# Kernel tuning notes

Measured on AMD Instinct MI355X. Metric: run time of the kernel, lower is better.

Reference implementation:

```python
import jax, jax.numpy as jnp
import numpy as np
from jax import lax

EPS = 1e-8

def int8_fq(x):
    # Int8ActPerTensorFloat: per-tensor float scale from runtime max-abs, fake-quant with STE.
    s = jnp.maximum(jnp.max(jnp.abs(x)) / 127.0, EPS)
    q = jnp.clip(jnp.round(x / s), -128.0, 127.0) * s
    return x + lax.stop_gradient(q - x)

def bin_w(w):
    # BINARY weight quant: per-tensor scale = mean(|w|), weights -> +/- scale (STE).
    s = jnp.mean(jnp.abs(w))
    wq = jnp.where(w >= 0, s, -s)
    return w + lax.stop_gradient(wq - w)

def qrelu(x):
    # QuantReLU with int8 input_quant and int8 act_quant
    return int8_fq(jax.nn.relu(int8_fq(x)))

def conv2d(x, w, b):
    y = lax.conv_general_dilated(x, w, window_strides=(1, 1), padding='VALID',
                                 dimension_numbers=('NCHW', 'OIHW', 'NCHW'))
    return y + b[None, :, None, None]

def maxpool2(x):
    return lax.reduce_window(x, -jnp.inf, lax.max, (1, 1, 2, 2), (1, 1, 2, 2), 'VALID')

def setup_inputs() -> dict:
    key = jax.random.key(0)
    ks = jax.random.split(key, 12)
    B = 16384
    inp = {
        'input_tensor': jax.random.normal(ks[0], (B, 3, 32, 32), dtype=jnp.float32),
        'w1': jax.random.normal(ks[1], (6, 3, 5, 5), dtype=jnp.float32) * 0.1,
        'b1': jax.random.normal(ks[2], (6,), dtype=jnp.float32) * 0.01,
        'w2': jax.random.normal(ks[3], (16, 6, 5, 5), dtype=jnp.float32) * 0.1,
        'b2': jax.random.normal(ks[4], (16,), dtype=jnp.float32) * 0.01,
        'fw1': jax.random.normal(ks[5], (120, 400), dtype=jnp.float32) * 0.05,
        'fb1': jax.random.normal(ks[6], (120,), dtype=jnp.float32) * 0.01,
        'fw2': jax.random.normal(ks[7], (84, 120), dtype=jnp.float32) * 0.05,
        'fb2': jax.random.normal(ks[8], (84,), dtype=jnp.float32) * 0.01,
        'fw3': jax.random.normal(ks[9], (10, 84), dtype=jnp.float32) * 0.05,
        'fb3': jax.random.normal(ks[10], (10,), dtype=jnp.float32) * 0.01,
    }
    return inp

def reference(input_tensor, w1, b1, w2, b2, fw1, fb1, fw2, fb2, fw3, fb3):
    x = int8_fq(input_tensor)                  # QuantIdentity
    x = qrelu(conv2d(x, bin_w(w1), b1))        # conv1 + relu1: [B,6,28,28]
    x = maxpool2(x)                            # [B,6,14,14]
    x = qrelu(conv2d(x, bin_w(w2), b2))        # conv2 + relu2: [B,16,10,10]
    x = maxpool2(x)                            # [B,16,5,5]
    x = x.reshape(x.shape[0], -1)              # [B,400]
    x = qrelu(x @ bin_w(fw1).T + fb1)          # fc1 + relu3: [B,120]
    x = qrelu(x @ bin_w(fw2).T + fb2)          # fc2 + relu4: [B,84]
    out = x @ bin_w(fw3).T + fb3               # fc3: [B,10]
    return out
```

## Files before the change

### kernel.cpp

```cpp
#include <hip/hip_runtime.h>
#include <math.h>

#define BATCH 16384
#define EPSQ 1e-8f

#define OFF_SCAL 0
#define OFF_WPK1 16
#define OFF_WPK2 196
#define OFF_FQ1  1156
#define OFF_FQ2  13156
#define OFF_FQ3  15844
#define OFF_A    16384
#define OFF_QIN   OFF_A
#define OFF_QC2   OFF_A
#define OFF_ISUM2 (OFF_A + 6400000)
#define OFF_QC3   (OFF_A + 10000000)
#define OFF_P3    (OFF_A + 12000000)
#define OFF_P4    (OFF_A + 14000000)
#define OFF_ISUM1 (OFF_A + 18874368)

__device__ inline int sdot4(unsigned int a, unsigned int b, int c) {
    return __builtin_amdgcn_sdot4((int)a, (int)b, c, false);
}

__device__ inline unsigned int fkey(float f) {
    unsigned int u = __float_as_uint(f);
    return (u & 0x80000000u) ? ~u : (u | 0x80000000u);
}
__device__ inline float fdec(unsigned int k) {
    unsigned int u = (k & 0x80000000u) ? (k ^ 0x80000000u) : ~k;
    return __uint_as_float(u);
}
#define KEY_ZERO   0x80000000u
#define KEY_NEGINF 0x007FFFFFu

__device__ inline float waveMax(float v) {
    #pragma unroll
    for (int off = 32; off > 0; off >>= 1)
        v = fmaxf(v, __shfl_down(v, off, 64));
    return v;
}

__device__ inline void blockAtomicMax2(float vmax, float vnmax,
                                       unsigned int* gmax, unsigned int* gnmax) {
    __shared__ float sm[4], sn[4];
    float a = waveMax(vmax), b = waveMax(vnmax);
    int tid = threadIdx.x;
    if ((tid & 63) == 0) { sm[tid >> 6] = a; sn[tid >> 6] = b; }
    __syncthreads();
    if (tid == 0) {
        atomicMax(gmax, fkey(fmaxf(fmaxf(sm[0], sm[1]), fmaxf(sm[2], sm[3]))));
        atomicMax(gnmax, fkey(fmaxf(fmaxf(sn[0], sn[1]), fmaxf(sn[2], sn[3]))));
    }
}

__device__ inline float fq_elem(float x, float s) {
    float q = fminf(fmaxf(rintf(x / s), -128.0f), 127.0f);
    return q * s;
}
__device__ inline int qrelu_code(float x, float s1, float s2) {
    float q = fq_elem(x, s1);
    q = fmaxf(q, 0.0f);
    return (int)fminf(fmaxf(rintf(q / s2), -128.0f), 127.0f);
}
__device__ inline void get_qrelu_scales(const unsigned int* scalu, int slot,
                                        float& s1, float& s2) {
    float maxa = fdec(scalu[slot]), negm = fdec(scalu[slot + 1]);
    float absm = fmaxf(maxa, negm);
    s1 = fmaxf(absm / 127.0f, EPSQ);
    float qm = fminf(fmaxf(rintf(maxa / s1), -128.0f), 127.0f) * s1;
    s2 = fmaxf(fmaxf(qm, 0.0f) / 127.0f, EPSQ);
}

__device__ inline unsigned int sgn8(float w) { return (w >= 0.0f) ? 0x01u : 0xFFu; }

__device__ inline unsigned int u32at(const unsigned int* wv, int wi, int k) {
    return (k == 0) ? wv[wi]
        : __builtin_amdgcn_perm(wv[wi + 1], wv[wi], 0x03020100u + 0x01010101u * (unsigned)k);
}

__global__ __launch_bounds__(256) void prep_kernel(const float* __restrict__ w1,
        const float* __restrict__ w2, const float* __restrict__ fw1,
        const float* __restrict__ fw2, const float* __restrict__ fw3,
        float* __restrict__ wsf) {
    int blk = blockIdx.x, tid = threadIdx.x;
    unsigned int* wsu = (unsigned int*)wsf;
    if (blk == 0) {
        if (tid == 0) wsu[0] = KEY_ZERO;
        else if (tid <= 8) wsu[tid] = KEY_NEGINF;
        return;
    }
    const float* src = nullptr; int N = 0;
    if (blk == 1)      { src = w1;  N = 450; }
    else if (blk == 2) { src = w2;  N = 2400; }
    else if (blk == 3) { src = fw1; N = 48000; }
    else if (blk == 4) { src = fw2; N = 10080; }
    else               { src = fw3; N = 840; }
    __shared__ float red[256];
    float partial = 0.0f;
    for (int i = tid; i < N; i += 256) partial += fabsf(src[i]);
    red[tid] = partial;
    __syncthreads();
    for (int s = 128; s > 0; s >>= 1) {
        if (tid < s) red[tid] += red[tid + s];
        __syncthreads();
    }
    if (tid == 0) wsf[8 + blk] = red[0] / (float)N;

    if (blk == 1) {
        for (int t = tid; t < 90; t += 256) {
            const float* wp = w1 + t * 5;
            wsu[OFF_WPK1 + 2*t] = sgn8(wp[0]) | (sgn8(wp[1])<<8) | (sgn8(wp[2])<<16) | (sgn8(wp[3])<<24);
            wsu[OFF_WPK1 + 2*t + 1] = sgn8(wp[4]) << 24;
        }
    } else if (blk == 2) {
        for (int t = tid; t < 480; t += 256) {
            const float* wp = w2 + t * 5;
            wsu[OFF_WPK2 + 2*t] = sgn8(wp[0]) | (sgn8(wp[1])<<8) | (sgn8(wp[2])<<16) | (sgn8(wp[3])<<24);
            wsu[OFF_WPK2 + 2*t + 1] = sgn8(wp[4]) << 24;
        }
    } else if (blk == 3) {
        for (int i = tid; i < 12000; i += 256) {
            int j = i / 100, k = i % 100;
            const float* wp = fw1 + j * 400 + k * 4;
            wsu[OFF_FQ1 + i] = sgn8(wp[0]) | (sgn8(wp[1])<<8) | (sgn8(wp[2])<<16) | (sgn8(wp[3])<<24);
        }
    } else if (blk == 4) {
        for (int i = tid; i < 2688; i += 256) {
            int j = i >> 5, k = i & 31;
            unsigned int u = 0;
            if (k < 30) {
                const float* wp = fw2 + j * 120 + k * 4;
                u = sgn8(wp[0]) | (sgn8(wp[1])<<8) | (sgn8(wp[2])<<16) | (sgn8(wp[3])<<24);
            }
            wsu[OFF_FQ2 + i] = u;
        }
    } else {
        for (int i = tid; i < 240; i += 256) {
            int j = i / 24, k = i % 24;
            unsigned int u = 0;
            if (k < 21) {
                const float* wp = fw3 + j * 84 + k * 4;
                u = sgn8(wp[0]) | (sgn8(wp[1])<<8) | (sgn8(wp[2])<<16) | (sgn8(wp[3])<<24);
            }
            wsu[OFF_FQ3 + i] = u;
        }
    }
}

__global__ __launch_bounds__(256) void absmax_kernel(const float4* __restrict__ x, int n4,
                                                     unsigned int* __restrict__ gkey) {
    float m = 0.0f;
    int stride = gridDim.x * 256;
    for (int i = blockIdx.x * 256 + threadIdx.x; i < n4; i += stride) {
        float4 v = x[i];
        m = fmaxf(m, fmaxf(fmaxf(fabsf(v.x), fabsf(v.y)), fmaxf(fabsf(v.z), fabsf(v.w))));
    }
    __shared__ float sm[4];
    m = waveMax(m);
    int tid = threadIdx.x;
    if ((tid & 63) == 0) sm[tid >> 6] = m;
    __syncthreads();
    if (tid == 0)
        atomicMax(gkey, fkey(fmaxf(fmaxf(sm[0], sm[1]), fmaxf(sm[2], sm[3]))));
}

__global__ __launch_bounds__(256) void quant1_kernel(const float4* __restrict__ x,
                                                     float* __restrict__ wsf) {
    unsigned int* wsu = (unsigned int*)wsf;
    float s0 = fmaxf(fdec(wsu[0]) / 127.0f, EPSQ);
    unsigned int* qin = wsu + OFF_QIN;
    int stride = gridDim.x * 256;
    const int total = BATCH * 96 * 12;
    for (int unit = blockIdx.x * 256 + threadIdx.x; unit < total; unit += stride) {
        int row_id = unit / 12, w = unit % 12;
        int plane = row_id >> 5, row = row_id & 31;
        int slot = (row >> 1) + ((row & 1) << 4);
        unsigned int u = 0;
        if (w < 8) {
            float4 v = x[row_id * 8 + w];
            int q0 = (int)fminf(fmaxf(rintf(v.x / s0), -128.f), 127.f);
            int q1 = (int)fminf(fmaxf(rintf(v.y / s0), -128.f), 127.f);
            int q2 = (int)fminf(fmaxf(rintf(v.z / s0), -128.f), 127.f);
            int q3 = (int)fminf(fmaxf(rintf(v.w / s0), -128.f), 127.f);
            u = (q0 & 255) | ((q1 & 255) << 8) | ((q2 & 255) << 16) | ((unsigned)(q3 & 255) << 24);
        }
        qin[(plane * 32 + slot) * 12 + w] = u;
    }
}

#define C1_ROWP 48
#define C1_CIS  1536
#define C1_IMGS 4608
#define C1_NIMG 12

template<int PH>
__device__ __forceinline__ void c1_phase(const unsigned char* ib, const unsigned int* wcp,
                                         int* ip, int& gmax, int& gmin) {
    int a0[14], a1[14];
    #pragma unroll
    for (int i = 0; i < 14; i++) { a0[i] = 0; a1[i] = 0; }
    #pragma unroll 1
    for (int ci = 0; ci < 3; ci++) {
        uint4 A[6]; unsigned int Bv[6];
        const unsigned char* cb = ib + ci * C1_CIS;
        #pragma unroll
        for (int r = 0; r < 6; r++) {
            const unsigned char* rb = cb + (((r & 1) << 4) + (r >> 1)) * C1_ROWP;
            if (PH == 0) {
                A[r]  = *(const uint4*)(rb);
                Bv[r] = *(const unsigned int*)(rb + 16);
            } else {
                Bv[r] = *(const unsigned int*)(rb + 12);
                A[r]  = *(const uint4*)(rb + 16);
            }
        }
        const unsigned int* wkp = wcp + ci * 10;
        unsigned int wk0[5], wk4[5];
        #pragma unroll
        for (int ky = 0; ky < 5; ky++) { wk0[ky] = wkp[2*ky]; wk4[ky] = wkp[2*ky+1]; }
        #pragma unroll
        for (int r6 = 0; r6 < 6; r6++) {
            unsigned int wv[5];
            if (PH == 0) {
                wv[0] = A[r6].x; wv[1] = A[r6].y; wv[2] = A[r6].z; wv[3] = A[r6].w; wv[4] = Bv[r6];
            } else {
                wv[0] = Bv[r6]; wv[1] = A[r6].x; wv[2] = A[r6].y; wv[3] = A[r6].z; wv[4] = A[r6].w;
            }
            const int OFS = (PH == 0) ? 0 : 2;
            unsigned int up[15];
            #pragma unroll
            for (int i = 0; i < 15; i++) {
                int e = OFS + i;
                up[i] = u32at(wv, e >> 2, e & 3);
            }
            if (r6 <= 4) {
                unsigned int w0 = wk0[r6], w4 = wk4[r6];
                #pragma unroll
                for (int i = 0; i < 14; i++) {
                    a0[i] = sdot4(up[i], w0, a0[i]);
                    a0[i] = sdot4(up[i+1], w4, a0[i]);
                }
            }
            if (r6 >= 1) {
                unsigned int w0 = wk0[r6-1], w4 = wk4[r6-1];
                #pragma unroll
                for (int i = 0; i < 14; i++) {
                    a1[i] = sdot4(up[i], w0, a1[i]);
                    a1[i] = sdot4(up[i+1], w4, a1[i]);
                }
            }
        }
    }
    #pragma unroll
    for (int i = 0; i < 14; i++) {
        gmax = max(gmax, max(a0[i], a1[i]));
        gmin = min(gmin, min(a0[i], a1[i]));
    }
    #pragma unroll
    for (int p = 0; p < 7; p++)
        ip[p] = max(max(a0[2*p], a0[2*p+1]), max(a1[2*p], a1[2*p+1]));
}

__global__ __launch_bounds__(256) void conv1_kernel(const float* __restrict__ b1,
                                                    float* __restrict__ wsf) {
    __shared__ __align__(16) unsigned char xq[C1_NIMG * C1_IMGS];
    __shared__ unsigned int wpk[180];
    __shared__ float bsm[6];
    unsigned int* wsu = (unsigned int*)wsf;
    int tid = threadIdx.x;
    int b0 = blockIdx.x * C1_NIMG;
    int nimg = min(C1_NIMG, BATCH - b0);
    float s0 = fmaxf(fdec(wsu[0]) / 127.0f, EPSQ);
    float seff = s0 * wsf[9];

    {
        const uint4* src = (const uint4*)((const unsigned char*)(wsu + OFF_QIN) + (size_t)b0 * C1_IMGS);
        uint4* dst = (uint4*)xq;
        for (int i = tid; i < nimg * 288; i += 256) dst[i] = src[i];
    }
    for (int i = tid; i < 180; i += 256) wpk[i] = wsu[OFF_WPK1 + i];
    if (tid < 6) bsm[tid] = b1[tid];
    __syncthreads();

    unsigned int* isum1 = wsu + OFF_ISUM1;
    float vmax = -INFINITY, vnmax = -INFINITY;
    int ntask = nimg * 84;
    for (int t = tid; t < ntask; t += 252) {
        if (tid >= 252) break;
        int img = t / 84, r = t % 84;
        int c = r / 14, py = r % 14;
        const unsigned char* ib = &xq[img * C1_IMGS + py * C1_ROWP];
        const unsigned int* wcp = &wpk[c * 30];
        int ip0[7], ip1[7];
        int gmax = -2000000000, gmin = 2000000000;
        c1_phase<0>(ib, wcp, ip0, gmax, gmin);
        c1_phase<1>(ib, wcp, ip1, gmax, gmin);
        float bias = bsm[c];
        vmax  = fmaxf(vmax,  fmaf(seff, (float)gmax, bias));
        vnmax = fmaxf(vnmax, -fmaf(seff, (float)gmin, bias));
        unsigned int* dst = isum1 + 588 * (size_t)(b0 + img) + 7 * (c * 14 + py);
        int v14[14];
        #pragma unroll
        for (int p = 0; p < 7; p++) { v14[p] = ip0[p]; v14[7 + p] = ip1[p]; }
        #pragma unroll
        for (int p = 0; p < 7; p++)
            dst[p] = (v14[2*p] & 0xFFFF) | ((unsigned)(v14[2*p+1] & 0xFFFF) << 16);
    }
    blockAtomicMax2(vmax, vnmax, wsu + 1, wsu + 2);
}

__global__ __launch_bounds__(256) void quant2_kernel(const float* __restrict__ b1,
                                                     float* __restrict__ wsf) {
    unsigned int* wsu = (unsigned int*)wsf;
    float s1, s2;
    get_qrelu_scales(wsu, 1, s1, s2);
    float s0 = fmaxf(fdec(wsu[0]) / 127.0f, EPSQ);
    float seff = s0 * wsf[9];
    float bv[6];
    #pragma unroll
    for (int c = 0; c < 6; c++) bv[c] = b1[c];
    const short* isum1 = (const short*)(wsu + OFF_ISUM1);
    unsigned int* qc2 = wsu + OFF_QC2;
    int stride = gridDim.x * 256;
    const int total = BATCH * 84 * 4;
    for (int unit = blockIdx.x * 256 + threadIdx.x; unit < total; unit += stride) {
        int row_id = unit >> 2, w = unit & 3;
        int bci = row_id / 14, row = row_id % 14;
        int ci = bci % 6;
        int slot = (row >> 1) + ((row & 1) << 3);
        float bias = bv[ci];
        unsigned int u = 0;
        const short* sp = isum1 + (size_t)bci * 196 + row * 14;
        #pragma unroll
        for (int k = 0; k < 4; k++) {
            int col = w * 4 + k;
            int code = 0;
            if (col < 14) {
                float pre = fmaf(seff, (float)sp[col], bias);
                code = qrelu_code(pre, s1, s2);
            }
            u |= ((unsigned)(code & 255)) << (8 * k);
        }
        qc2[((size_t)bci * 16 + slot) * 4 + w] = u;
    }
}

#define C2_ROWP 16
#define C2_CIS  256
#define C2_IMGS 1536
#define C2_NIMG 16

__global__ __launch_bounds__(256) void conv2_kernel(const float* __restrict__ b2,
                                                    float* __restrict__ wsf) {
    __shared__ __align__(16) unsigned char act[C2_NIMG * C2_IMGS];
    __shared__ unsigned int wpk[960];
    __shared__ float bsm[16];
    __shared__ __align__(16) short spb[C2_NIMG * 400];
    unsigned int* wsu = (unsigned int*)wsf;
    int tid = threadIdx.x;
    int b0 = blockIdx.x * C2_NIMG;
    float s1, s2;
    get_qrelu_scales(wsu, 1, s1, s2);
    float seff = s2 * wsf[10];

    {
        const uint4* src = (const uint4*)((const unsigned char*)(wsu + OFF_QC2) + (size_t)b0 * C2_IMGS);
        uint4* dst = (uint4*)act;
        for (int i = tid; i < C2_NIMG * 96; i += 256) dst[i] = src[i];
    }
    for (int i = tid; i < 960; i += 256) wpk[i] = wsu[OFF_WPK2 + i];
    if (tid < 16) bsm[tid] = b2[tid];
    __syncthreads();

    float vmax = -INFINITY, vnmax = -INFINITY;
    const int ntask = C2_NIMG * 80;
    for (int t = tid; t < ntask; t += 256) {
        int img = t / 80, r = t % 80;
        int c = r / 5, py = r % 5;
        const unsigned char* ib = &act[img * C2_IMGS + py * C2_ROWP];
        int a0[10], a1[10];
        #pragma unroll
        for (int i = 0; i < 10; i++) { a0[i] = 0; a1[i] = 0; }
        #pragma unroll 1
        for (int cig = 0; cig < 3; cig++) {
            uint4 R[2][6];
            #pragma unroll
            for (int g = 0; g < 2; g++)
                #pragma unroll
                for (int r6 = 0; r6 < 6; r6++)
                    R[g][r6] = *(const uint4*)(ib + (2*cig + g) * C2_CIS
                                + (((r6 & 1) << 3) + (r6 >> 1)) * C2_ROWP);
            #pragma unroll
            for (int g = 0; g < 2; g++) {
                int ci = 2*cig + g;
                const unsigned int* wkp = &wpk[(c * 6 + ci) * 10];
                unsigned int wk0[5], wk4[5];
                #pragma unroll
                for (int ky = 0; ky < 5; ky++) { wk0[ky] = wkp[2*ky]; wk4[ky] = wkp[2*ky+1]; }
                #pragma unroll
                for (int r6 = 0; r6 < 6; r6++) {
                    unsigned int wv[4] = { R[g][r6].x, R[g][r6].y, R[g][r6].z, R[g][r6].w };
                    unsigned int up[11];
                    #pragma unroll
                    for (int i = 0; i < 11; i++) up[i] = u32at(wv, i >> 2, i & 3);
                    if (r6 <= 4) {
                        unsigned int w0 = wk0[r6], w4 = wk4[r6];
                        #pragma unroll
                        for (int i = 0; i < 10; i++) {
                            a0[i] = sdot4(up[i], w0, a0[i]);
                            a0[i] = sdot4(up[i+1], w4, a0[i]);
                        }
                    }
                    if (r6 >= 1) {
                        unsigned int w0 = wk0[r6-1], w4 = wk4[r6-1];
                        #pragma unroll
                        for (int i = 0; i < 10; i++) {
                            a1[i] = sdot4(up[i], w0, a1[i]);
                            a1[i] = sdot4(up[i+1], w4, a1[i]);
                        }
                    }
                }
            }
        }
        int gmax = -2000000000, gmin = 2000000000;
        #pragma unroll
        for (int i = 0; i < 10; i++) {
            gmax = max(gmax, max(a0[i], a1[i]));
            gmin = min(gmin, min(a0[i], a1[i]));
        }
        float bias = bsm[c];
        vmax  = fmaxf(vmax,  fmaf(seff, (float)gmax, bias));
        vnmax = fmaxf(vnmax, -fmaf(seff, (float)gmin, bias));
        short* dst = spb + img * 400 + c * 25 + py * 5;
        #pragma unroll
        for (int p = 0; p < 5; p++)
            dst[p] = (short)max(max(a0[2*p], a0[2*p+1]), max(a1[2*p], a1[2*p+1]));
    }
    __syncthreads();
    {
        const uint4* pb4 = (const uint4*)spb;
        uint4* d4 = (uint4*)((short*)(wsu + OFF_ISUM2) + (size_t)b0 * 400);
        for (int i = tid; i < C2_NIMG * 50; i += 256) d4[i] = pb4[i];
    }
    blockAtomicMax2(vmax, vnmax, wsu + 3, wsu + 4);
}

__global__ __launch_bounds__(256) void quant3_kernel(const float* __restrict__ b2,
                                                     float* __restrict__ wsf) {
    unsigned int* wsu = (unsigned int*)wsf;
    float s1, s2;
    get_qrelu_scales(wsu, 3, s1, s2);
    float sp1, sp2;
    get_qrelu_scales(wsu, 1, sp1, sp2);
    float seff = sp2 * wsf[10];
    __shared__ float bv[16];
    if (threadIdx.x < 16) bv[threadIdx.x] = b2[threadIdx.x];
    __syncthreads();
    const short* isum2 = (const short*)(wsu + OFF_ISUM2);
    unsigned int* qc3 = wsu + OFF_QC3;
    int stride = gridDim.x * 256;
    const int total = BATCH * 100;
    for (int unit = blockIdx.x * 256 + threadIdx.x; unit < total; unit += stride) {
        int b = unit / 100, w = unit % 100;
        const short* sp = isum2 + (size_t)b * 400 + w * 4;
        unsigned int u = 0;
        #pragma unroll
        for (int k = 0; k < 4; k++) {
            int p = w * 4 + k;
            float pre = fmaf(seff, (float)sp[k], bv[p / 25]);
            int code = qrelu_code(pre, s1, s2);
            u |= ((unsigned)(code & 255)) << (8 * k);
        }
        qc3[unit] = u;
    }
}

__global__ __launch_bounds__(256) void fc1_kernel(const float* __restrict__ fb1,
                                                  float* __restrict__ wsf) {
    __shared__ unsigned int xs[32][100];
    __shared__ __align__(16) float pb[32 * 120];
    unsigned int* wsu = (unsigned int*)wsf;
    float* p3 = wsf + OFF_P3;
    int tid = threadIdx.x;
    size_t row0 = (size_t)blockIdx.x * 32;
    float s1, s2;
    get_qrelu_scales(wsu, 3, s1, s2);
    float seff = s2 * wsf[11];
    {
        const uint4* src = (const uint4*)(wsu + OFF_QC3 + row0 * 100);
        uint4* dst = (uint4*)xs;
        for (int i = tid; i < 800; i += 256) dst[i] = src[i];
    }
    __syncthreads();
    float vmax = -INFINITY, vnmax = -INFINITY;
    if (tid < 240) {
        int g = tid / 120, j = tid % 120;
        int acc[16];
        #pragma unroll
        for (int r = 0; r < 16; r++) acc[r] = 0;
        const uint4* wrow = (const uint4*)&wsu[OFF_FQ1 + j * 100];
        for (int kg = 0; kg < 25; kg++) {
            uint4 wv = wrow[kg];
            #pragma unroll
            for (int r = 0; r < 16; r++) {
                uint4 xv = *(const uint4*)&xs[g * 16 + r][kg * 4];
                acc[r] = sdot4(xv.x, wv.x, acc[r]);
                acc[r] = sdot4(xv.y, wv.y, acc[r]);
                acc[r] = sdot4(xv.z, wv.z, acc[r]);
                acc[r] = sdot4(xv.w, wv.w, acc[r]);
            }
        }
        float bias = fb1[j];
        #pragma unroll
        for (int r = 0; r < 16; r++) {
            float pv = fmaf(seff, (float)acc[r], bias);
            pb[(g * 16 + r) * 120 + j] = pv;
            vmax = fmaxf(vmax, pv); vnmax = fmaxf(vnmax, -pv);
        }
    }
    __syncthreads();
    {
        const float4* pb4 = (const float4*)pb;
        float4* d4 = (float4*)(p3 + row0 * 120);
        for (int i = tid; i < 960; i += 256) d4[i] = pb4[i];
    }
    blockAtomicMax2(vmax, vnmax, wsu + 5, wsu + 6);
}

__global__ __launch_bounds__(256) void fc2_kernel(const float* __restrict__ fb2,
                                                  float* __restrict__ wsf) {
    __shared__ unsigned int xs[48][32];
    __shared__ __align__(16) float pb[48 * 84];
    unsigned int* wsu = (unsigned int*)wsf;
    const float* p3 = wsf + OFF_P3;
    float* p4 = wsf + OFF_P4;
    int tid = threadIdx.x;
    size_t row0 = (size_t)blockIdx.x * 48;
    int nrow = min(48, (int)(BATCH - row0));
    float s1, s2;
    get_qrelu_scales(wsu, 5, s1, s2);
    float seff = s2 * wsf[12];
    const float4* src = (const float4*)(p3 + row0 * 120);
    for (int i = tid; i < nrow * 30; i += 256) {
        float4 v = src[i];
        int c0 = qrelu_code(v.x, s1, s2), c1 = qrelu_code(v.y, s1, s2);
        int c2 = qrelu_code(v.z, s1, s2), c3 = qrelu_code(v.w, s1, s2);
        xs[i / 30][i % 30] = c0 | (c1 << 8) | (c2 << 16) | ((unsigned)c3 << 24);
    }
    if (tid < 48) { xs[tid][30] = 0; xs[tid][31] = 0; }
    __syncthreads();
    float vmax = -INFINITY, vnmax = -INFINITY;
    if (tid < 252) {
        int g = tid / 84, j = tid % 84;
        int acc[16];
        #pragma unroll
        for (int r = 0; r < 16; r++) acc[r] = 0;
        const uint4* wrow = (const uint4*)&wsu[OFF_FQ2 + j * 32];
        #pragma unroll
        for (int kg = 0; kg < 8; kg++) {
            uint4 wv = wrow[kg];
            #pragma unroll
            for (int r = 0; r < 16; r++) {
                uint4 xv = *(const uint4*)&xs[g * 16 + r][kg * 4];
                acc[r] = sdot4(xv.x, wv.x, acc[r]);
                acc[r] = sdot4(xv.y, wv.y, acc[r]);
                acc[r] = sdot4(xv.z, wv.z, acc[r]);
                acc[r] = sdot4(xv.w, wv.w, acc[r]);
            }
        }
        float bias = fb2[j];
        #pragma unroll
        for (int r = 0; r < 16; r++) {
            int lr = g * 16 + r;
            if (lr < nrow) {
                float pv = fmaf(seff, (float)acc[r], bias);
                pb[lr * 84 + j] = pv;
                vmax = fmaxf(vmax, pv); vnmax = fmaxf(vnmax, -pv);
            }
        }
    }
    __syncthreads();
    {
        const float4* pb4 = (const float4*)pb;
        float4* d4 = (float4*)(p4 + row0 * 84);
        for (int i = tid; i < nrow * 21; i += 256) d4[i] = pb4[i];
    }
    blockAtomicMax2(vmax, vnmax, wsu + 7, wsu + 8);
}

__global__ __launch_bounds__(256) void fc3_kernel(const float* __restrict__ fb3,
                                                  float* __restrict__ out,
                                                  float* __restrict__ wsf) {
    __shared__ unsigned int wsm[240];
    __shared__ float bs[10];
    __shared__ __align__(16) float pb[2560];
    unsigned int* wsu = (unsigned int*)wsf;
    const float* p4 = wsf + OFF_P4;
    int tid = threadIdx.x;
    for (int i = tid; i < 240; i += 256) wsm[i] = wsu[OFF_FQ3 + i];
    if (tid < 10) bs[tid] = fb3[tid];
    __syncthreads();
    float s1, s2;
    get_qrelu_scales(wsu, 7, s1, s2);
    float seff = s2 * wsf[13];
    size_t row = (size_t)blockIdx.x * 256 + tid;
    unsigned int xr[24];
    const float4* src = (const float4*)(p4 + row * 84);
    #pragma unroll
    for (int k = 0; k < 21; k++) {
        float4 v = src[k];
        int c0 = qrelu_code(v.x, s1, s2), c1 = qrelu_code(v.y, s1, s2);
        int c2 = qrelu_code(v.z, s1, s2), c3 = qrelu_code(v.w, s1, s2);
        xr[k] = c0 | (c1 << 8) | (c2 << 16) | ((unsigned)c3 << 24);
    }
    xr[21] = 0; xr[22] = 0; xr[23] = 0;
    #pragma unroll
    for (int j = 0; j < 10; j++) {
        int acc = 0;
        #pragma unroll
        for (int k = 0; k < 24; k++) acc = sdot4(xr[k], wsm[j * 24 + k], acc);
        pb[tid * 10 + j] = fmaf(seff, (float)acc, bs[j]);
    }
    __syncthreads();
    {
        const float4* pb4 = (const float4*)pb;
        float4* d4 = (float4*)(out + (size_t)blockIdx.x * 2560);
        for (int i = tid; i < 640; i += 256) d4[i] = pb4[i];
    }
}

extern "C" void kernel_launch(void* const* d_in, const int* in_sizes, int n_in,
                              void* d_out, int out_size, void* d_ws, size_t ws_size,
                              hipStream_t stream) {
    const float* input = (const float*)d_in[0];
    const float* w1  = (const float*)d_in[1];
    const float* b1  = (const float*)d_in[2];
    const float* w2  = (const float*)d_in[3];
    const float* b2  = (const float*)d_in[4];
    const float* fw1 = (const float*)d_in[5];
    const float* fb1 = (const float*)d_in[6];
    const float* fw2 = (const float*)d_in[7];
    const float* fb2 = (const float*)d_in[8];
    const float* fw3 = (const float*)d_in[9];
    const float* fb3 = (const float*)d_in[10];
    float* ws  = (float*)d_ws;
    float* out = (float*)d_out;

    prep_kernel<<<6, 256, 0, stream>>>(w1, w2, fw1, fw2, fw3, ws);
    absmax_kernel<<<2048, 256, 0, stream>>>((const float4*)input,
                                            (int)((size_t)BATCH * 3072 / 4),
                                            (unsigned int*)ws);
    quant1_kernel<<<8192, 256, 0, stream>>>((const float4*)input, ws);
    conv1_kernel<<<(BATCH + C1_NIMG - 1) / C1_NIMG, 256, 0, stream>>>(b1, ws);
    quant2_kernel<<<4096, 256, 0, stream>>>(b1, ws);
    conv2_kernel<<<BATCH / C2_NIMG, 256, 0, stream>>>(b2, ws);
    quant3_kernel<<<2048, 256, 0, stream>>>(b2, ws);
    fc1_kernel<<<BATCH / 32, 256, 0, stream>>>(fb1, ws);
    fc2_kernel<<<(BATCH + 47) / 48, 256, 0, stream>>>(fb2, ws);
    fc3_kernel<<<BATCH / 256, 256, 0, stream>>>(fb3, out, ws);
}
```

Baseline: 467.6 us.

## Compute multiple output channels per thread in conv1 and conv2 for input reuse

```diff
diff --git a/kernel.cpp b/kernel.cpp
--- a/kernel.cpp
+++ b/kernel.cpp
@@ -192,14 +192,16 @@
 #define C1_ROWP 48
 #define C1_CIS  1536
 #define C1_IMGS 4608
-#define C1_NIMG 12
+#define C1_NIMG 9
 
 template<int PH>
-__device__ __forceinline__ void c1_phase(const unsigned char* ib, const unsigned int* wcp,
-                                         int* ip, int& gmax, int& gmin) {
-    int a0[14], a1[14];
+__device__ __forceinline__ void c1_phase3(const unsigned char* ib, const unsigned int* wcp,
+                                          int ip[3][7], int gmax[3], int gmin[3]) {
+    int a0[3][14], a1[3][14];
     #pragma unroll
-    for (int i = 0; i < 14; i++) { a0[i] = 0; a1[i] = 0; }
+    for (int cc = 0; cc < 3; cc++)
+        #pragma unroll
+        for (int i = 0; i < 14; i++) { a0[cc][i] = 0; a1[cc][i] = 0; }
     #pragma unroll 1
     for (int ci = 0; ci < 3; ci++) {
         uint4 A[6]; unsigned int Bv[6];
@@ -215,10 +217,6 @@
                 A[r]  = *(const uint4*)(rb + 16);
             }
         }
-        const unsigned int* wkp = wcp + ci * 10;
-        unsigned int wk0[5], wk4[5];
-        #pragma unroll
-        for (int ky = 0; ky < 5; ky++) { wk0[ky] = wkp[2*ky]; wk4[ky] = wkp[2*ky+1]; }
         #pragma unroll
         for (int r6 = 0; r6 < 6; r6++) {
             unsigned int wv[5];
@@ -234,32 +232,39 @@
                 int e = OFS + i;
                 up[i] = u32at(wv, e >> 2, e & 3);
             }
-            if (r6 <= 4) {
-                unsigned int w0 = wk0[r6], w4 = wk4[r6];
-                #pragma unroll
-                for (int i = 0; i < 14; i++) {
-                    a0[i] = sdot4(up[i], w0, a0[i]);
-                    a0[i] = sdot4(up[i+1], w4, a0[i]);
+            #pragma unroll
+            for (int cc = 0; cc < 3; cc++) {
+                const unsigned int* wkp = wcp + cc * 30 + ci * 10;
+                if (r6 <= 4) {
+                    unsigned int w0 = wkp[2 * r6], w4 = wkp[2 * r6 + 1];
+                    #pragma unroll
+                    for (int i = 0; i < 14; i++) {
+                        a0[cc][i] = sdot4(up[i], w0, a0[cc][i]);
+                        a0[cc][i] = sdot4(up[i + 1], w4, a0[cc][i]);
+                    }
                 }
-            }
-            if (r6 >= 1) {
-                unsigned int w0 = wk0[r6-1], w4 = wk4[r6-1];
-                #pragma unroll
-                for (int i = 0; i < 14; i++) {
-                    a1[i] = sdot4(up[i], w0, a1[i]);
-                    a1[i] = sdot4(up[i+1], w4, a1[i]);
+                if (r6 >= 1) {
+                    unsigned int w0 = wkp[2 * (r6 - 1)], w4 = wkp[2 * (r6 - 1) + 1];
+                    #pragma unroll
+                    for (int i = 0; i < 14; i++) {
+                        a1[cc][i] = sdot4(up[i], w0, a1[cc][i]);
+                        a1[cc][i] = sdot4(up[i + 1], w4, a1[cc][i]);
+                    }
                 }
             }
         }
     }
     #pragma unroll
-    for (int i = 0; i < 14; i++) {
-        gmax = max(gmax, max(a0[i], a1[i]));
-        gmin = min(gmin, min(a0[i], a1[i]));
-    }
-    #pragma unroll
-    for (int p = 0; p < 7; p++)
-        ip[p] = max(max(a0[2*p], a0[2*p+1]), max(a1[2*p], a1[2*p+1]));
+    for (int cc = 0; cc < 3; cc++) {
+        #pragma unroll
+        for (int i = 0; i < 14; i++) {
+            gmax[cc] = max(gmax[cc], max(a0[cc][i], a1[cc][i]));
+            gmin[cc] = min(gmin[cc], min(a0[cc][i], a1[cc][i]));
+        }
+        #pragma unroll
+        for (int p = 0; p < 7; p++)
+            ip[cc][p] = max(max(a0[cc][2*p], a0[cc][2*p+1]), max(a1[cc][2*p], a1[cc][2*p+1]));
+    }
 }
 
 __global__ __launch_bounds__(256) void conv1_kernel(const float* __restrict__ b1,
@@ -285,27 +290,31 @@
 
     unsigned int* isum1 = wsu + OFF_ISUM1;
     float vmax = -INFINITY, vnmax = -INFINITY;
-    int ntask = nimg * 84;
-    for (int t = tid; t < ntask; t += 252) {
-        if (tid >= 252) break;
-        int img = t / 84, r = t % 84;
-        int c = r / 14, py = r % 14;
+    int ntask = nimg * 28;
+    if (tid < ntask) {
+        int img = tid / 28, rem = tid % 28;
+        int chalf = rem / 14, py = rem % 14;
+        int c0 = chalf * 3;
         const unsigned char* ib = &xq[img * C1_IMGS + py * C1_ROWP];
-        const unsigned int* wcp = &wpk[c * 30];
-        int ip0[7], ip1[7];
-        int gmax = -2000000000, gmin = 2000000000;
-        c1_phase<0>(ib, wcp, ip0, gmax, gmin);
-        c1_phase<1>(ib, wcp, ip1, gmax, gmin);
-        float bias = bsm[c];
-        vmax  = fmaxf(vmax,  fmaf(seff, (float)gmax, bias));
-        vnmax = fmaxf(vnmax, -fmaf(seff, (float)gmin, bias));
-        unsigned int* dst = isum1 + 588 * (size_t)(b0 + img) + 7 * (c * 14 + py);
-        int v14[14];
-        #pragma unroll
-        for (int p = 0; p < 7; p++) { v14[p] = ip0[p]; v14[7 + p] = ip1[p]; }
-        #pragma unroll
-        for (int p = 0; p < 7; p++)
-            dst[p] = (v14[2*p] & 0xFFFF) | ((unsigned)(v14[2*p+1] & 0xFFFF) << 16);
+        const unsigned int* wcp = &wpk[c0 * 30];
+        int ip0[3][7], ip1[3][7];
+        int gmax[3] = {-2000000000, -2000000000, -2000000000};
+        int gmin[3] = { 2000000000,  2000000000,  2000000000};
+        c1_phase3<0>(ib, wcp, ip0, gmax, gmin);
+        c1_phase3<1>(ib, wcp, ip1, gmax, gmin);
+        #pragma unroll
+        for (int cc = 0; cc < 3; cc++) {
+            float bias = bsm[c0 + cc];
+            vmax  = fmaxf(vmax,  fmaf(seff, (float)gmax[cc], bias));
+            vnmax = fmaxf(vnmax, -fmaf(seff, (float)gmin[cc], bias));
+            unsigned int* dst = isum1 + 588 * (size_t)(b0 + img) + 7 * ((c0 + cc) * 14 + py);
+            int v14[14];
+            #pragma unroll
+            for (int p = 0; p < 7; p++) { v14[p] = ip0[cc][p]; v14[7 + p] = ip1[cc][p]; }
+            #pragma unroll
+            for (int p = 0; p < 7; p++)
+                dst[p] = (v14[2*p] & 0xFFFF) | ((unsigned)(v14[2*p+1] & 0xFFFF) << 16);
+        }
     }
     blockAtomicMax2(vmax, vnmax, wsu + 1, wsu + 2);
 }
@@ -349,7 +358,7 @@
 #define C2_ROWP 16
 #define C2_CIS  256
 #define C2_IMGS 1536
-#define C2_NIMG 16
+#define C2_NIMG 12
 
 __global__ __launch_bounds__(256) void conv2_kernel(const float* __restrict__ b2,
                                                     float* __restrict__ wsf) {
@@ -360,6 +369,7 @@
     unsigned int* wsu = (unsigned int*)wsf;
     int tid = threadIdx.x;
     int b0 = blockIdx.x * C2_NIMG;
+    int nimg = min(C2_NIMG, BATCH - b0);
     float s1, s2;
     get_qrelu_scales(wsu, 1, s1, s2);
     float seff = s2 * wsf[10];
@@ -367,81 +377,81 @@
     {
         const uint4* src = (const uint4*)((const unsigned char*)(wsu + OFF_QC2) + (size_t)b0 * C2_IMGS);
         uint4* dst = (uint4*)act;
-        for (int i = tid; i < C2_NIMG * 96; i += 256) dst[i] = src[i];
+        for (int i = tid; i < nimg * 96; i += 256) dst[i] = src[i];
     }
     for (int i = tid; i < 960; i += 256) wpk[i] = wsu[OFF_WPK2 + i];
     if (tid < 16) bsm[tid] = b2[tid];
     __syncthreads();
 
     float vmax = -INFINITY, vnmax = -INFINITY;
-    const int ntask = C2_NIMG * 80;
-    for (int t = tid; t < ntask; t += 256) {
-        int img = t / 80, r = t % 80;
-        int c = r / 5, py = r % 5;
+    int ntask = nimg * 20;
+    if (tid < ntask) {
+        int img = tid / 20, rem = tid % 20;
+        int cq = rem / 5, py = rem % 5;
+        int c0 = cq * 4;
         const unsigned char* ib = &act[img * C2_IMGS + py * C2_ROWP];
-        int a0[10], a1[10];
-        #pragma unroll
-        for (int i = 0; i < 10; i++) { a0[i] = 0; a1[i] = 0; }
+        int a0[4][10], a1[4][10];
+        #pragma unroll
+        for (int cc = 0; cc < 4; cc++)
+            #pragma unroll
+            for (int i = 0; i < 10; i++) { a0[cc][i] = 0; a1[cc][i] = 0; }
         #pragma unroll 1
-        for (int cig = 0; cig < 3; cig++) {
-            uint4 R[2][6];
-            #pragma unroll
-            for (int g = 0; g < 2; g++)
+        for (int ci = 0; ci < 6; ci++) {
+            uint4 R[6];
+            #pragma unroll
+            for (int r6 = 0; r6 < 6; r6++)
+                R[r6] = *(const uint4*)(ib + ci * C2_CIS + (((r6 & 1) << 3) + (r6 >> 1)) * C2_ROWP);
+            #pragma unroll
+            for (int r6 = 0; r6 < 6; r6++) {
+                unsigned int wv[4] = { R[r6].x, R[r6].y, R[r6].z, R[r6].w };
+                unsigned int up[11];
                 #pragma unroll
-                for (int r6 = 0; r6 < 6; r6++)
-                    R[g][r6] = *(const uint4*)(ib + (2*cig + g) * C2_CIS
-                                + (((r6 & 1) << 3) + (r6 >> 1)) * C2_ROWP);
-            #pragma unroll
-            for (int g = 0; g < 2; g++) {
-                int ci = 2*cig + g;
-                const unsigned int* wkp = &wpk[(c * 6 + ci) * 10];
-                unsigned int wk0[5], wk4[5];
+                for (int i = 0; i < 11; i++) up[i] = u32at(wv, i >> 2, i & 3);
                 #pragma unroll
-                for (int ky = 0; ky < 5; ky++) { wk0[ky] = wkp[2*ky]; wk4[ky] = wkp[2*ky+1]; }
-                #pragma unroll
-                for (int r6 = 0; r6 < 6; r6++) {
-                    unsigned int wv[4] = { R[g][r6].x, R[g][r6].y, R[g][r6].z, R[g][r6].w };
-                    unsigned int up[11];
-                    #pragma unroll
-                    for (int i = 0; i < 11; i++) up[i] = u32at(wv, i >> 2, i & 3);
+                for (int cc = 0; cc < 4; cc++) {
+                    const unsigned int* wkp = &wpk[((c0 + cc) * 6 + ci) * 10];
                     if (r6 <= 4) {
-                        unsigned int w0 = wk0[r6], w4 = wk4[r6];
+                        unsigned int w0 = wkp[2 * r6], w4 = wkp[2 * r6 + 1];
                         #pragma unroll
                         for (int i = 0; i < 10; i++) {
-                            a0[i] = sdot4(up[i], w0, a0[i]);
-                            a0[i] = sdot4(up[i+1], w4, a0[i]);
+                            a0[cc][i] = sdot4(up[i], w0, a0[cc][i]);
+                            a0[cc][i] = sdot4(up[i + 1], w4, a0[cc][i]);
                         }
                     }
                     if (r6 >= 1) {
-                        unsigned int w0 = wk0[r6-1], w4 = wk4[r6-1];
+                        unsigned int w0 = wkp[2 * (r6 - 1)], w4 = wkp[2 * (r6 - 1) + 1];
                         #pragma unroll
                         for (int i = 0; i < 10; i++) {
-                            a1[i] = sdot4(up[i], w0, a1[i]);
-                            a1[i] = sdot4(up[i+1], w4, a1[i]);
+                            a1[cc][i] = sdot4(up[i], w0, a1[cc][i]);
+                            a1[cc][i] = sdot4(up[i + 1], w4, a1[cc][i]);
                         }
                     }
                 }
             }
         }
-        int gmax = -2000000000, gmin = 2000000000;
-        #pragma unroll
-        for (int i = 0; i < 10; i++) {
-            gmax = max(gmax, max(a0[i], a1[i]));
-            gmin = min(gmin, min(a0[i], a1[i]));
-        }
-        float bias = bsm[c];
-        vmax  = fmaxf(vmax,  fmaf(seff, (float)gmax, bias));
-        vnmax = fmaxf(vnmax, -fmaf(seff, (float)gmin, bias));
-        short* dst = spb + img * 400 + c * 25 + py * 5;
-        #pragma unroll
-        for (int p = 0; p < 5; p++)
-            dst[p] = (short)max(max(a0[2*p], a0[2*p+1]), max(a1[2*p], a1[2*p+1]));
+        #pragma unroll
+        for (int cc = 0; cc < 4; cc++) {
+            int gmax = -2000000000, gmin = 2000000000;
+            #pragma unroll
+            for (int i = 0; i < 10; i++) {
+                gmax = max(gmax, max(a0[cc][i], a1[cc][i]));
+                gmin = min(gmin, min(a0[cc][i], a1[cc][i]));
+            }
+            float bias = bsm[c0 + cc];
+            vmax  = fmaxf(vmax,  fmaf(seff, (float)gmax, bias));
+            vnmax = fmaxf(vnmax, -fmaf(seff, (float)gmin, bias));
+            short* dst = spb + img * 400 + (c0 + cc) * 25 + py * 5;
+            #pragma unroll
+            for (int p = 0; p < 5; p++)
+                dst[p] = (short)max(max(a0[cc][2*p], a0[cc][2*p+1]),
+                                    max(a1[cc][2*p], a1[cc][2*p+1]));
+        }
     }
     __syncthreads();
     {
         const uint4* pb4 = (const uint4*)spb;
         uint4* d4 = (uint4*)((short*)(wsu + OFF_ISUM2) + (size_t)b0 * 400);
-        for (int i = tid; i < C2_NIMG * 50; i += 256) d4[i] = pb4[i];
+        for (int i = tid; i < nimg * 50; i += 256) d4[i] = pb4[i];
     }
     blockAtomicMax2(vmax, vnmax, wsu + 3, wsu + 4);
 }
@@ -654,7 +664,7 @@
     quant1_kernel<<<8192, 256, 0, stream>>>((const float4*)input, ws);
     conv1_kernel<<<(BATCH + C1_NIMG - 1) / C1_NIMG, 256, 0, stream>>>(b1, ws);
     quant2_kernel<<<4096, 256, 0, stream>>>(b1, ws);
-    conv2_kernel<<<BATCH / C2_NIMG, 256, 0, stream>>>(b2, ws);
+    conv2_kernel<<<(BATCH + C2_NIMG - 1) / C2_NIMG, 256, 0, stream>>>(b2, ws);
     quant3_kernel<<<2048, 256, 0, stream>>>(b2, ws);
     fc1_kernel<<<BATCH / 32, 256, 0, stream>>>(fb1, ws);
     fc2_kernel<<<(BATCH + 47) / 48, 256, 0, stream>>>(fb2, ws);
```

Result: no change. 465.5 us (median of 2 runs) (-0.4%).
